# Performance work log

Hardware: AMD Instinct MI355X
Metric: run time of the kernel (lower is better)

Reference implementation:

```python
import jax, jax.numpy as jnp
import numpy as np

BS, N_PER, EMBED, ENC, L, OUT = 8, 8192, 128, 512, 512, 256
N = BS * N_PER          # total batched nodes
E_PER = 131072          # edges per graph (avg degree 16)
N_HE = 4096             # number of hyperedges (global over batched graph)
P = 1048576             # hyperedge incidence pairs


def _lin(k, i, o):
    return (jax.random.normal(k, (i, o), jnp.float32) / np.sqrt(i)).astype(jnp.float32)


def setup_inputs() -> dict:
    key = jax.random.key(0)
    ks = jax.random.split(key, 16)
    x = jax.random.normal(ks[0], (BS, L, ENC), jnp.float32)
    node_features = jax.random.normal(ks[1], (BS, N_PER, EMBED), jnp.float32)
    # block-diagonal batched graph (dgl.batch semantics): edges stay within each graph
    off = (jnp.arange(BS, dtype=jnp.int32) * N_PER)[:, None]
    src = (jax.random.randint(ks[2], (BS, E_PER), 0, N_PER) + off).reshape(-1)
    dst = (jax.random.randint(ks[3], (BS, E_PER), 0, N_PER) + off).reshape(-1)
    edge_index = jnp.stack([src, dst])                      # [2, E]
    hn = jax.random.randint(ks[4], (P,), 0, N)              # incident node ids
    he = jax.random.randint(ks[5], (P,), 0, N_HE)           # incident hyperedge ids
    hyperedge_index = jnp.stack([hn, he], axis=1)           # [P, 2], transposed in forward like the torch code
    return {
        "x": x, "node_features": node_features,
        "edge_index": edge_index, "hyperedge_index": hyperedge_index,
        "Wg1": _lin(ks[6], EMBED, EMBED), "bg1": jnp.zeros((EMBED,), jnp.float32),
        "Wg2": _lin(ks[7], EMBED, EMBED), "bg2": jnp.zeros((EMBED,), jnp.float32),
        "Wh1": _lin(ks[8], EMBED, EMBED), "bh1": jnp.zeros((EMBED,), jnp.float32),
        "Wh2": _lin(ks[9], EMBED, EMBED), "bh2": jnp.zeros((EMBED,), jnp.float32),
        "Wm": _lin(ks[10], ENC, EMBED), "bm": jnp.zeros((EMBED,), jnp.float32),
        "Wm2": _lin(ks[11], EMBED, EMBED), "bm2": jnp.zeros((EMBED,), jnp.float32),
        "Ws": _lin(ks[12], ENC + EMBED, OUT // 2), "bs_": jnp.zeros((OUT // 2,), jnp.float32),
        "Wt": _lin(ks[13], ENC + EMBED, OUT // 2), "bt": jnp.zeros((OUT // 2,), jnp.float32),
    }


def _gconv(h, src, dst, W, b):
    # DGL GraphConv, norm='both', allow_zero_in_degree (degrees clamped to 1)
    ones = jnp.ones(src.shape, h.dtype)
    dout = jnp.maximum(jax.ops.segment_sum(ones, src, num_segments=N), 1.0)
    din = jnp.maximum(jax.ops.segment_sum(ones, dst, num_segments=N), 1.0)
    h = h * jax.lax.rsqrt(dout)[:, None]
    h = h @ W
    agg = jax.ops.segment_sum(h[src], dst, num_segments=N)
    return agg * jax.lax.rsqrt(din)[:, None] + b


def _hconv(h, pn, pe, W, b):
    # PyG HypergraphConv with hyperedge_weight=None (ones): X' = D^-1 H B^-1 H^T (X Theta) + bias
    h = h @ W
    ones = jnp.ones(pn.shape, h.dtype)
    D = jax.ops.segment_sum(ones, pn, num_segments=N)       # node hyper-degree
    B = jax.ops.segment_sum(ones, pe, num_segments=N_HE)    # hyperedge size
    Dinv = jnp.where(D > 0, 1.0 / D, 0.0)
    Binv = jnp.where(B > 0, 1.0 / B, 0.0)
    ef = Binv[:, None] * jax.ops.segment_sum(h[pn], pe, num_segments=N_HE)
    out = Dinv[:, None] * jax.ops.segment_sum(ef[pe], pn, num_segments=N)
    return out + b


def reference(x, node_features, edge_index, hyperedge_index,
              Wg1, bg1, Wg2, bg2, Wh1, bh1, Wh2, bh2,
              Wm, bm, Wm2, bm2, Ws, bs_, Wt, bt):
    src, dst = edge_index[0], edge_index[1]
    hidx = hyperedge_index.T                 # matches torch .transpose(0, 1)
    pn, pe = hidx[0], hidx[1]
    nfr = node_features.reshape(N, EMBED)    # concatenated per-graph node features

    h = _gconv(nfr, src, dst, Wg1, bg1)
    h = _hconv(h, pn, pe, Wh1, bh1)
    h = jax.nn.relu(h) + nfr
    h = _gconv(h, src, dst, Wg2, bg2)
    h = _hconv(h, pn, pe, Wh2, bh2)
    h = jax.nn.relu(h) + nfr

    g = h.reshape(BS, N_PER, EMBED)          # equal node counts -> pad/split is a reshape
    q = jax.nn.relu(x @ Wm + bm)             # [BS, L, EMBED]
    k = jax.nn.relu(jnp.einsum('bnd,de->bne', g, Wm2) + bm2)
    C = jnp.einsum('bld,bnd->bln', q, k)     # cross-attention scores
    H = jnp.einsum('bln,bnd->bld', jax.nn.softmax(C, axis=2), g)
    cat = jnp.concatenate([x, H], axis=2)    # [BS, L, ENC+EMBED]
    G1 = jax.nn.sigmoid(cat @ Ws + bs_)
    G2 = jnp.tanh(cat @ Wt + bt)
    return jnp.concatenate([G1, G2], axis=2)  # [BS, L, OUT], dropout is identity at eval
```

## Files before the change

kernel.cpp:

```cpp
#include <hip/hip_runtime.h>
#include <hip/hip_bf16.h>

#define BSZ   8
#define NPER  8192
#define NNODE 65536
#define EPG   131072
#define EMB   128
#define ENCD  512
#define LQ    512
#define NHE   4096
#define NE    1048576
#define NP    1048576
#define NROW  4096
#define NSPLIT 16
#define SLOT_N 64
#define SLOT_E 384
#define CAP_E  10240
#define CAP_PN 10240
#define CAP_PE 18432

typedef _Float16 f16;
typedef _Float16 f16x2 __attribute__((ext_vector_type(2)));
typedef _Float16 f16x4 __attribute__((ext_vector_type(4)));
typedef _Float16 f16x8 __attribute__((ext_vector_type(8)));
typedef float f32x4 __attribute__((ext_vector_type(4)));
typedef unsigned short u16;
typedef unsigned int u32;

__global__ __launch_bounds__(256) void k_bin(const int* __restrict__ eidx,
    const int* __restrict__ hidx, int* __restrict__ gcur,
    u32* __restrict__ bin_e, u32* __restrict__ bin_s,
    u32* __restrict__ bin_pn, u32* __restrict__ bin_pe)
{
  __shared__ int lh[448];
  __shared__ int gb[448];
  const int tid = threadIdx.x;
  for (int i = tid; i < 448; i += 256) lh[i] = 0;
  __syncthreads();
  if (blockIdx.x < 256){
    const int eb4 = blockIdx.x*1024;
    int ss[16], dd[16];
    #pragma unroll
    for (int t = 0; t < 4; ++t){
      int4 s4 = ((const int4*)eidx)[eb4 + t*256 + tid];
      int4 d4 = ((const int4*)(eidx + NE))[eb4 + t*256 + tid];
      ss[t*4+0]=s4.x; ss[t*4+1]=s4.y; ss[t*4+2]=s4.z; ss[t*4+3]=s4.w;
      dd[t*4+0]=d4.x; dd[t*4+1]=d4.y; dd[t*4+2]=d4.z; dd[t*4+3]=d4.w;
    }
    int rd[16], rs[16];
    #pragma unroll
    for (int u = 0; u < 16; ++u){
      rd[u] = atomicAdd(&lh[dd[u] >> 9], 1);
      rs[u] = atomicAdd(&lh[128 + (ss[u] >> 9)], 1);
    }
    __syncthreads();
    if (tid < 128){
      if (lh[tid]) gb[tid] = atomicAdd(&gcur[tid], lh[tid]);
    } else {
      if (lh[tid]) gb[tid] = atomicAdd(&gcur[192 + tid], lh[tid]);
    }
    __syncthreads();
    #pragma unroll
    for (int u = 0; u < 16; ++u){
      int b = dd[u] >> 9;
      int pos = gb[b] + rd[u];
      if (pos < CAP_E)
        bin_e[(size_t)b*CAP_E + pos] = (u32)(dd[u] & 0xffff) | ((u32)ss[u] << 16);
      int bs = ss[u] >> 9;
      int pos2 = gb[128 + bs] + rs[u];
      if (pos2 < CAP_E)
        bin_s[(size_t)bs*CAP_E + pos2] = (u32)(ss[u] & 0xffff);
    }
  } else {
    const int pb4 = (blockIdx.x - 256)*2048;
    int pn[16], pe[16];
    #pragma unroll
    for (int t = 0; t < 8; ++t){
      int4 p = ((const int4*)hidx)[pb4 + t*256 + tid];
      pn[t*2+0] = p.x; pe[t*2+0] = p.y;
      pn[t*2+1] = p.z; pe[t*2+1] = p.w;
    }
    int rn[16], re[16];
    #pragma unroll
    for (int u = 0; u < 16; ++u){
      rn[u] = atomicAdd(&lh[128 + (pn[u] >> 9)], 1);
      re[u] = atomicAdd(&lh[256 + (pe[u] >> 6)], 1);
    }
    __syncthreads();
    if (tid < 192 && lh[128 + tid]) gb[128 + tid] = atomicAdd(&gcur[128 + tid], lh[128 + tid]);
    __syncthreads();
    #pragma unroll
    for (int u = 0; u < 16; ++u){
      int bn = pn[u] >> 9;
      int pos = gb[128 + bn] + rn[u];
      if (pos < CAP_PN)
        bin_pn[(size_t)bn*CAP_PN + pos] = (u32)pn[u] | ((u32)pe[u] << 16);
      int be = pe[u] >> 6;
      int pos2 = gb[256 + be] + re[u];
      if (pos2 < CAP_PE)
        bin_pe[(size_t)be*CAP_PE + pos2] = (u32)pe[u] | ((u32)pn[u] << 16);
    }
  }
}

__global__ __launch_bounds__(256) void k_csr(const int* __restrict__ gcur,
    const u32* __restrict__ bin_e, const u32* __restrict__ bin_s,
    const u32* __restrict__ bin_pn, const u32* __restrict__ bin_pe,
    int* __restrict__ cnt_dst, u16* __restrict__ csr_dst,
    int* __restrict__ cnt_pn, u16* __restrict__ csr_pn,
    int* __restrict__ cnt_pe, u16* __restrict__ csr_pe,
    int* __restrict__ du)
{
  const int tid = threadIdx.x;
  if (blockIdx.x < 256){
    __shared__ int cur[512];
    const int isP = blockIdx.x >= 128;
    const int b = blockIdx.x & 127;
    cur[tid] = 0; cur[tid + 256] = 0;
    __syncthreads();
    const int n0 = b*512;
    const int cap = isP ? CAP_PN : CAP_E;
    int raw = gcur[isP ? 128 + b : b];
    int count = raw < cap ? raw : cap;
    const u32* bin = (isP ? bin_pn : bin_e) + (size_t)b*cap;
    u16* csr = isP ? csr_pn : csr_dst;
    for (int i = tid; i < count; i += 256){
      u32 v = bin[i];
      int row = v & 0xffff, val = v >> 16;
      int c = atomicAdd(&cur[row - n0], 1);
      if (c < SLOT_N) csr[(size_t)row*SLOT_N + c] = (u16)val;
    }
    __syncthreads();
    int* cnt = isP ? cnt_pn : cnt_dst;
    cnt[n0 + tid]       = cur[tid];
    cnt[n0 + 256 + tid] = cur[tid + 256];
  } else if (blockIdx.x < 320){
    __shared__ int cur[64];
    const int b = blockIdx.x - 256;
    if (tid < 64) cur[tid] = 0;
    __syncthreads();
    const int e0 = b*64;
    int raw = gcur[256 + b];
    int count = raw < CAP_PE ? raw : CAP_PE;
    const u32* bin = bin_pe + (size_t)b*CAP_PE;
    for (int i = tid; i < count; i += 256){
      u32 v = bin[i];
      int row = v & 0xffff, val = v >> 16;
      int c = atomicAdd(&cur[row - e0], 1);
      if (c < SLOT_E) csr_pe[(size_t)row*SLOT_E + c] = (u16)val;
    }
    __syncthreads();
    if (tid < 64) cnt_pe[e0 + tid] = cur[tid];
  } else {
    __shared__ int cur[512];
    const int b = blockIdx.x - 320;
    cur[tid] = 0; cur[tid + 256] = 0;
    __syncthreads();
    const int n0 = b*512;
    int raw = gcur[320 + b];
    int count = raw < CAP_E ? raw : CAP_E;
    const u32* bin = bin_s + (size_t)b*CAP_E;
    for (int i = tid; i < count; i += 256){
      int row = (int)(bin[i] & 0xffff);
      atomicAdd(&cur[row - n0], 1);
    }
    __syncthreads();
    du[n0 + tid]       = cur[tid];
    du[n0 + 256 + tid] = cur[tid + 256];
  }
}

__global__ __launch_bounds__(256) void k_wprep(const float* __restrict__ Wg1,
    const float* __restrict__ Wg2, const float* __restrict__ Wm2,
    f16* __restrict__ wg1, f16* __restrict__ wg2, f16* __restrict__ wm2)
{
  int id = blockIdx.x*256 + threadIdx.x;
  int wsel = id >> 12;
  int r = id & 4095;
  int n = r >> 5, k0 = (r & 31)*4;
  const float* src = (wsel == 0 ? Wg1 : wsel == 1 ? Wg2 : Wm2) + n;
  f16* dst = wsel == 0 ? wg1 : wsel == 1 ? wg2 : wm2;
  f16x4 o = { (f16)src[(k0+0)*128], (f16)src[(k0+1)*128],
              (f16)src[(k0+2)*128], (f16)src[(k0+3)*128] };
  *(f16x4*)(dst + n*128 + k0) = o;
}

__global__ __launch_bounds__(256) void k_pre(const float* __restrict__ nfr,
    const int* __restrict__ du, f16* __restrict__ out)
{
  int i = blockIdx.x*256 + threadIdx.x;
  int node = i >> 6, j = i & 63;
  float ds = rsqrtf(fmaxf((float)du[node], 1.f));
  float2 v = ((const float2*)(nfr + (size_t)node*128))[j];
  f16x2 o = { (f16)(v.x*ds), (f16)(v.y*ds) };
  ((f16x2*)(out + (size_t)node*128))[j] = o;
}

__global__ __launch_bounds__(256) void k_gagg16(const int* __restrict__ cnt,
    const u16* __restrict__ csr, const f16* __restrict__ src, f16* __restrict__ agg)
{
  const int wv = threadIdx.x >> 6, lane = threadIdx.x & 63;
  const int blk = blockIdx.x;
  const int n = (blk & 7)*NPER + (blk >> 3)*4 + wv;
  const int nd = cnt[n];
  const int c = nd < SLOT_N ? nd : SLOT_N;
  const u16* row = csr + (size_t)n*SLOT_N;
  const f16x2* s2 = (const f16x2*)src;
  float ax = 0.f, ay = 0.f;
  if (c > 0){
    const int i0 = row[0];
    #pragma unroll 1
    for (int b = 0; b < 8; ++b){
      if (b*8 >= c) break;
      int4 iv = *(const int4*)(row + b*8);
      int ix[8] = { iv.x & 0xffff, (iv.x >> 16) & 0xffff,
                    iv.y & 0xffff, (iv.y >> 16) & 0xffff,
                    iv.z & 0xffff, (iv.z >> 16) & 0xffff,
                    iv.w & 0xffff, (iv.w >> 16) & 0xffff };
      f16x2 vv[8];
      #pragma unroll
      for (int k = 0; k < 8; ++k){
        int id = (b*8 + k < c) ? ix[k] : i0;
        vv[k] = s2[(size_t)id*64 + lane];
      }
      #pragma unroll
      for (int k = 0; k < 8; ++k){
        if (b*8 + k < c){ ax += (float)vv[k].x; ay += (float)vv[k].y; }
      }
    }
  }
  ((f16x2*)(agg + (size_t)n*128))[lane] = (f16x2){ (f16)ax, (f16)ay };
}

__global__ __launch_bounds__(256) void k_hea16(const int* __restrict__ cnt,
    const u16* __restrict__ csr, const f16* __restrict__ src, float* __restrict__ ef)
{
  const int wv = threadIdx.x >> 6, lane = threadIdx.x & 63;
  const int e = blockIdx.x*4 + wv;
  const int nd = cnt[e];
  const int n = nd < SLOT_E ? nd : SLOT_E;
  const u16* row = csr + (size_t)e*SLOT_E;
  const f16x2* s2 = (const f16x2*)src;
  float ax = 0.f, ay = 0.f;
  int j = 0;
  for (; j + 7 < n; j += 8){
    int p0 = row[j],   p1 = row[j+1], p2 = row[j+2], p3 = row[j+3];
    int p4 = row[j+4], p5 = row[j+5], p6 = row[j+6], p7 = row[j+7];
    f16x2 v0 = s2[(size_t)p0*64 + lane];
    f16x2 v1 = s2[(size_t)p1*64 + lane];
    f16x2 v2 = s2[(size_t)p2*64 + lane];
    f16x2 v3 = s2[(size_t)p3*64 + lane];
    f16x2 v4 = s2[(size_t)p4*64 + lane];
    f16x2 v5 = s2[(size_t)p5*64 + lane];
    f16x2 v6 = s2[(size_t)p6*64 + lane];
    f16x2 v7 = s2[(size_t)p7*64 + lane];
    ax += (((float)v0.x + (float)v1.x) + ((float)v2.x + (float)v3.x))
        + (((float)v4.x + (float)v5.x) + ((float)v6.x + (float)v7.x));
    ay += (((float)v0.y + (float)v1.y) + ((float)v2.y + (float)v3.y))
        + (((float)v4.y + (float)v5.y) + ((float)v6.y + (float)v7.y));
  }
  for (; j < n; ++j){
    f16x2 v = s2[(size_t)row[j]*64 + lane];
    ax += (float)v.x; ay += (float)v.y;
  }
  float s = nd > 0 ? 1.f/(float)nd : 0.f;
  ((float2*)(ef + (size_t)e*128))[lane] = make_float2(ax*s, ay*s);
}

template<int MODE>
__global__ __launch_bounds__(256) void k_ngemm(const f16* __restrict__ inp,
    const f16* __restrict__ wT, const int* __restrict__ cnt,
    const float* __restrict__ bias, f16* __restrict__ outp)
{
  const int wv = threadIdx.x >> 6, lane = threadIdx.x & 63;
  const int quad = lane >> 4, col = lane & 15;
  const int koff = quad*8;
  const int row0 = blockIdx.x*64 + wv*16;
  const f16* ar = inp + (size_t)(row0 + col)*128 + koff;
  const f16* br = wT + (size_t)col*128 + koff;
  f32x4 acc[8];
  #pragma unroll
  for (int nt = 0; nt < 8; ++nt) acc[nt] = (f32x4){0.f,0.f,0.f,0.f};
  #pragma unroll
  for (int ks = 0; ks < 4; ++ks){
    f16x8 a = *(const f16x8*)(ar + ks*32);
    #pragma unroll
    for (int nt = 0; nt < 8; ++nt){
      f16x8 b = *(const f16x8*)(br + (size_t)nt*16*128 + ks*32);
      acc[nt] = __builtin_amdgcn_mfma_f32_16x16x32_f16(a, b, acc[nt], 0, 0, 0);
    }
  }
  float sc[4];
  #pragma unroll
  for (int r = 0; r < 4; ++r)
    sc[r] = (MODE == 1) ? rsqrtf(fmaxf((float)cnt[row0 + quad*4 + r], 1.f)) : 1.f;
  #pragma unroll
  for (int nt = 0; nt < 8; ++nt){
    int n = nt*16 + col;
    float bv = bias[n];
    #pragma unroll
    for (int r = 0; r < 4; ++r){
      float v = acc[nt][r];
      if (MODE == 1) v = v*sc[r] + bv;
      else           v = fmaxf(v + bv, 0.f);
      outp[(size_t)(row0 + quad*4 + r)*128 + n] = (f16)v;
    }
  }
}

template<int MODE, int IN16>
__global__ __launch_bounds__(256, 2) void k_gemm(const void* __restrict__ inp,
    const float* __restrict__ W, const int* __restrict__ cnt,
    const float* __restrict__ bias, void* __restrict__ outp)
{
  __shared__ float Wl[128*128];
  __shared__ float Rl[32*128];
  const int tid = threadIdx.x;
  const int rbase = blockIdx.x*32;
  for (int i = tid; i < 16384; i += 256) Wl[i] = W[i];
  if (IN16){
    const f16x2* s2 = (const f16x2*)(((const f16*)inp) + (size_t)rbase*128);
    for (int i = tid; i < 2048; i += 256){
      f16x2 v = s2[i];
      ((float2*)Rl)[i] = make_float2((float)v.x, (float)v.y);
    }
  } else {
    const float* src = ((const float*)inp) + (size_t)rbase*128;
    for (int i = tid; i < 4096; i += 256) Rl[i] = src[i];
  }
  __syncthreads();
  const int c0 = (tid & 31)*4;
  const int r0 = (tid >> 5)*4;
  f32x4 acc[4];
  #pragma unroll
  for (int j = 0; j < 4; ++j) acc[j] = (f32x4){0.f,0.f,0.f,0.f};
  for (int d = 0; d < 128; d += 4){
    f32x4 w0 = *(const f32x4*)&Wl[(d+0)*128 + c0];
    f32x4 w1 = *(const f32x4*)&Wl[(d+1)*128 + c0];
    f32x4 w2 = *(const f32x4*)&Wl[(d+2)*128 + c0];
    f32x4 w3 = *(const f32x4*)&Wl[(d+3)*128 + c0];
    #pragma unroll
    for (int j = 0; j < 4; ++j){
      f32x4 rr = *(const f32x4*)&Rl[(r0+j)*128 + d];
      acc[j] += rr.x*w0 + rr.y*w1 + rr.z*w2 + rr.w*w3;
    }
  }
  #pragma unroll
  for (int j = 0; j < 4; ++j){
    const int row = rbase + r0 + j;
    if (MODE == 0){
      *(f32x4*)(((float*)outp) + (size_t)row*128 + c0) = acc[j];
    } else if (MODE == 1){
      float sc = rsqrtf(fmaxf((float)cnt[row], 1.f));
      f16* o = ((f16*)outp) + (size_t)row*128 + c0;
      #pragma unroll
      for (int k = 0; k < 4; ++k) o[k] = (f16)(acc[j][k]*sc + bias[c0+k]);
    } else if (MODE == 2){
      f16* o = ((f16*)outp) + (size_t)row*128 + c0;
      #pragma unroll
      for (int k = 0; k < 4; ++k) o[k] = (f16)fmaxf(acc[j][k] + bias[c0+k], 0.f);
    } else {
      f16* o = ((f16*)outp) + (size_t)row*128 + c0;
      #pragma unroll
      for (int k = 0; k < 4; ++k) o[k] = (f16)acc[j][k];
    }
  }
}

template<int PRES>
__global__ __launch_bounds__(256) void k_nha(const int* __restrict__ cnt,
    const u16* __restrict__ csr, const f16* __restrict__ ef,
    const float* __restrict__ bias, const float* __restrict__ nfr,
    const int* __restrict__ du, f16* __restrict__ outp)
{
  const int wv = threadIdx.x >> 6, lane = threadIdx.x & 63;
  const int n = blockIdx.x*4 + wv;
  const int nd = cnt[n];
  const int c = nd < SLOT_N ? nd : SLOT_N;
  const u16* row = csr + (size_t)n*SLOT_N;
  const f16x2* s2 = (const f16x2*)ef;
  float2 nf = ((const float2*)(nfr + (size_t)n*128))[lane];
  float e0 = PRES ? rsqrtf(fmaxf((float)du[n], 1.f)) : 1.f;
  float ax = 0.f, ay = 0.f;
  if (c > 0){
    const int i0 = row[0];
    #pragma unroll 1
    for (int b = 0; b < 8; ++b){
      if (b*8 >= c) break;
      int4 iv = *(const int4*)(row + b*8);
      int ix[8] = { iv.x & 0xffff, (iv.x >> 16) & 0xffff,
                    iv.y & 0xffff, (iv.y >> 16) & 0xffff,
                    iv.z & 0xffff, (iv.z >> 16) & 0xffff,
                    iv.w & 0xffff, (iv.w >> 16) & 0xffff };
      f16x2 vv[8];
      #pragma unroll
      for (int k = 0; k < 8; ++k){
        int id = (b*8 + k < c) ? ix[k] : i0;
        vv[k] = s2[(size_t)id*64 + lane];
      }
      #pragma unroll
      for (int k = 0; k < 8; ++k){
        if (b*8 + k < c){ ax += (float)vv[k].x; ay += (float)vv[k].y; }
      }
    }
  }
  float bx = bias[lane*2], by = bias[lane*2+1];
  float s = nd > 0 ? 1.f/(float)nd : 0.f;
  float vx = fmaxf(ax*s + bx, 0.f) + nf.x;
  float vy = fmaxf(ay*s + by, 0.f) + nf.y;
  ((f16x2*)(outp + (size_t)n*128))[lane] = (f16x2){ (f16)(vx*e0), (f16)(vy*e0) };
}

__global__ __launch_bounds__(256) void k_gt(const f16* __restrict__ g, f16* __restrict__ gT)
{
  __shared__ f16 t[64][66];
  int b = blockIdx.z, n0 = blockIdx.x*64, c0 = blockIdx.y*64;
  for (int i = threadIdx.x; i < 64*64; i += 256){
    int n = i >> 6, c = i & 63;
    t[n][c] = g[((size_t)(b*NPER + n0 + n))*128 + c0 + c];
  }
  __syncthreads();
  for (int i = threadIdx.x; i < 64*64; i += 256){
    int c = i >> 6, n = i & 63;
    gT[((size_t)(b*128 + c0 + c))*NPER + n0 + n] = t[n][c];
  }
}

#define NCH 64
__global__ __launch_bounds__(512, 4) void k_flash(const f16* __restrict__ qb,
    const f16* __restrict__ kb, const f16* __restrict__ gT,
    f16* __restrict__ Opart, float* __restrict__ mZ)
{
  __shared__ f16 Kl[64*128];
  __shared__ f16 Vl[128*64];
  __shared__ f16 Pl[8*16*64];
  const int sp = blockIdx.x, l0 = blockIdx.y*128, b = blockIdx.z;
  const int tid = threadIdx.x;
  const int w = tid >> 6, lane = tid & 63;
  const int quad = lane >> 4, col = lane & 15;
  const int koff = quad*8;
  const int krow = tid >> 4;
  const int kc8  = tid & 15;
  const int vrow = tid >> 3;
  const int vc8  = tid & 7;

  const f16* qrow = qb + ((size_t)(b*LQ + l0 + w*16 + col))*128 + koff;
  f16x8 aq[4];
  #pragma unroll
  for (int ks = 0; ks < 4; ++ks) aq[ks] = *(const f16x8*)(qrow + ks*32);
  float mrun[4] = {-1e30f,-1e30f,-1e30f,-1e30f};
  float zrun[4] = {0.f,0.f,0.f,0.f};
  f32x4 O[8];
  #pragma unroll
  for (int i = 0; i < 8; ++i) O[i] = (f32x4){0.f,0.f,0.f,0.f};

  const int nbase = sp*(NPER/NSPLIT);
  f16x8 kr[2], vr[2];
#define LOADKV(N0)                                                           \
  { _Pragma("unroll")                                                        \
    for (int i2 = 0; i2 < 2; ++i2){                                          \
      kr[i2] = *(const f16x8*)(kb + ((size_t)(b*NPER + (N0) + krow + i2*32))*128 + kc8*8); \
      vr[i2] = *(const f16x8*)(gT + ((size_t)(b*128 + vrow + i2*64))*NPER + (N0) + vc8*8); \
    } }
  LOADKV(nbase);
  #pragma unroll 1
  for (int it = 0; it < (NPER/NSPLIT)/NCH; ++it){
    const int n0 = nbase + it*NCH;
    __syncthreads();
    #pragma unroll
    for (int i2 = 0; i2 < 2; ++i2){
      int r = krow + i2*32;
      *(f16x8*)&Kl[r*128 + ((kc8 ^ (r & 7))*8)] = kr[i2];
      int d = vrow + i2*64;
      *(f16x8*)&Vl[d*64  + ((vc8 ^ (d & 7))*8)] = vr[i2];
    }
    __syncthreads();
    if (it < (NPER/NSPLIT)/NCH - 1) LOADKV(n0 + NCH);

    f32x4 st[4];
    #pragma unroll
    for (int t = 0; t < 4; ++t){
      st[t] = (f32x4){0.f,0.f,0.f,0.f};
      const int r = t*16 + col, rs = r & 7;
      #pragma unroll
      for (int ks = 0; ks < 4; ++ks){
        f16x8 bf = *(const f16x8*)&Kl[r*128 + (((ks*4 + quad) ^ rs)*8)];
        st[t] = __builtin_amdgcn_mfma_f32_16x16x32_f16(aq[ks], bf, st[t], 0, 0, 0);
      }
    }
    float alr[4];
    #pragma unroll
    for (int r = 0; r < 4; ++r){
      float rm = st[0][r];
      #pragma unroll
      for (int t = 1; t < 4; ++t) rm = fmaxf(rm, st[t][r]);
      rm = fmaxf(rm, __shfl_xor(rm, 1));
      rm = fmaxf(rm, __shfl_xor(rm, 2));
      rm = fmaxf(rm, __shfl_xor(rm, 4));
      rm = fmaxf(rm, __shfl_xor(rm, 8));
      float mn = fmaxf(mrun[r], rm);
      float al = __expf(mrun[r] - mn);
      float ps[4], rsum = 0.f;
      #pragma unroll
      for (int t = 0; t < 4; ++t){ ps[t] = __expf(st[t][r] - mn); rsum += ps[t]; }
      rsum += __shfl_xor(rsum, 1);
      rsum += __shfl_xor(rsum, 2);
      rsum += __shfl_xor(rsum, 4);
      rsum += __shfl_xor(rsum, 8);
      zrun[r] = zrun[r]*al + rsum;
      mrun[r] = mn;
      alr[r] = al;
      const int prow = quad*4 + r, pswz = prow & 7;
      #pragma unroll
      for (int t = 0; t < 4; ++t)
        Pl[w*1024 + prow*64 + (((t*2 + (col >> 3)) ^ pswz)*8) + (col & 7)] = (f16)ps[t];
    }
    #pragma unroll
    for (int dt = 0; dt < 8; ++dt)
      #pragma unroll
      for (int r = 0; r < 4; ++r) O[dt][r] *= alr[r];
    __builtin_amdgcn_wave_barrier();
    #pragma unroll
    for (int kk = 0; kk < 2; ++kk){
      f16x8 ap = *(const f16x8*)&Pl[w*1024 + col*64 + (((kk*4 + quad) ^ (col & 7))*8)];
      #pragma unroll
      for (int dt = 0; dt < 8; ++dt){
        const int d = col + dt*16;
        f16x8 bv = *(const f16x8*)&Vl[d*64 + (((kk*4 + quad) ^ (d & 7))*8)];
        O[dt] = __builtin_amdgcn_mfma_f32_16x16x32_f16(ap, bv, O[dt], 0, 0, 0);
      }
    }
    __builtin_amdgcn_wave_barrier();
  }
#undef LOADKV
  const int growb = b*LQ + l0 + w*16 + quad*4;
  #pragma unroll
  for (int r = 0; r < 4; ++r){
    f16* od = Opart + ((size_t)sp*NROW + growb + r)*128 + col;
    #pragma unroll
    for (int dt = 0; dt < 8; ++dt) od[dt*16] = (f16)O[dt][r];
  }
  if (col == 0){
    #pragma unroll
    for (int r = 0; r < 4; ++r){
      ((float2*)mZ)[(size_t)sp*NROW + growb + r] = make_float2(mrun[r], zrun[r]);
    }
  }
}

__global__ __launch_bounds__(256) void k_comb(const f16* __restrict__ Opart,
    const float* __restrict__ mZ, f16* __restrict__ cat)
{
  int i = blockIdx.x*256 + threadIdx.x;
  int row = i >> 6, d2 = (i & 63)*2;
  float ms[NSPLIT], zs[NSPLIT];
  float M = -1e30f;
  #pragma unroll
  for (int s = 0; s < NSPLIT; ++s){
    float2 v = ((const float2*)mZ)[(size_t)s*NROW + row];
    ms[s] = v.x; zs[s] = v.y;
    M = fmaxf(M, v.x);
  }
  float Zt = 0.f, ax = 0.f, ay = 0.f;
  #pragma unroll
  for (int s = 0; s < NSPLIT; ++s){
    float e = __expf(ms[s] - M);
    Zt += zs[s]*e;
    f16x2 op = *(const f16x2*)(Opart + ((size_t)s*NROW + row)*128 + d2);
    ax += e*(float)op.x; ay += e*(float)op.y;
  }
  float inv = 1.f/Zt;
  f16x2 o = { (f16)(ax*inv), (f16)(ay*inv) };
  *(f16x2*)(cat + (size_t)row*640 + 512 + d2) = o;
}

__global__ __launch_bounds__(256) void k_prep(const float* __restrict__ x,
    const float* __restrict__ Wsg, const float* __restrict__ Wtn,
    const float* __restrict__ Wm,
    f16* __restrict__ cat, f16* __restrict__ w16, f16* __restrict__ wm16)
{
  if (blockIdx.x < 2048){
    int id = blockIdx.x*256 + threadIdx.x;
    int row = id >> 7, c4 = (id & 127)*4;
    float4 v = *(const float4*)(x + (size_t)row*512 + c4);
    f16x4 o = { (f16)v.x, (f16)v.y, (f16)v.z, (f16)v.w };
    *(f16x4*)(cat + (size_t)row*640 + c4) = o;
  } else if (blockIdx.x < 2208){
    int id = (blockIdx.x - 2048)*256 + threadIdx.x;
    int n = id / 160;
    int k0 = (id - n*160)*4;
    const float* src = n < 128 ? (Wsg + n) : (Wtn + (n - 128));
    f16x4 o = { (f16)src[(k0+0)*128], (f16)src[(k0+1)*128],
                (f16)src[(k0+2)*128], (f16)src[(k0+3)*128] };
    *(f16x4*)(w16 + (size_t)n*640 + k0) = o;
  } else {
    int id = (blockIdx.x - 2208)*256 + threadIdx.x;
    int n = id >> 7;
    int k0 = (id & 127)*4;
    const float* src = Wm + n;
    f16x4 o = { (f16)src[(k0+0)*128], (f16)src[(k0+1)*128],
                (f16)src[(k0+2)*128], (f16)src[(k0+3)*128] };
    *(f16x4*)(wm16 + (size_t)n*512 + k0) = o;
  }
}

__global__ __launch_bounds__(64) void k_qgemm2(const f16* __restrict__ cat,
    const f16* __restrict__ wm16, const float* __restrict__ bm, f16* __restrict__ q)
{
  const int lane = threadIdx.x;
  const int quad = lane >> 4, col = lane & 15;
  const int koff = quad*8;
  const int row0 = blockIdx.x * 16;
  const f16* ar = cat + (size_t)(row0 + col)*640 + koff;
  const f16* br = wm16 + (size_t)col*512 + koff;
  f32x4 acc[8];
  #pragma unroll
  for (int nt = 0; nt < 8; ++nt) acc[nt] = (f32x4){0.f,0.f,0.f,0.f};
  for (int ks = 0; ks < 16; ++ks){
    f16x8 a = *(const f16x8*)(ar + ks*32);
    #pragma unroll
    for (int nt = 0; nt < 8; ++nt){
      f16x8 b = *(const f16x8*)(br + (size_t)nt*16*512 + ks*32);
      acc[nt] = __builtin_amdgcn_mfma_f32_16x16x32_f16(a, b, acc[nt], 0, 0, 0);
    }
  }
  #pragma unroll
  for (int nt = 0; nt < 8; ++nt){
    int n = nt*16 + col;
    float bv = bm[n];
    #pragma unroll
    for (int r = 0; r < 4; ++r){
      float v = fmaxf(acc[nt][r] + bv, 0.f);
      q[(size_t)(row0 + quad*4 + r)*128 + n] = (f16)v;
    }
  }
}

__global__ __launch_bounds__(64) void k_fin2(const f16* __restrict__ cat,
    const f16* __restrict__ w16, const float* __restrict__ bsg,
    const float* __restrict__ btn, float* __restrict__ out)
{
  const int lane = threadIdx.x;
  const int quad = lane >> 4, col = lane & 15;
  const int koff = quad*8;
  const int row0 = blockIdx.x * 16;
  const f16* ar = cat + (size_t)(row0 + col)*640 + koff;
  const f16* br = w16 + (size_t)col*640 + koff;
  f32x4 acc[16];
  #pragma unroll
  for (int nt = 0; nt < 16; ++nt) acc[nt] = (f32x4){0.f,0.f,0.f,0.f};
  for (int ks = 0; ks < 20; ++ks){
    f16x8 a = *(const f16x8*)(ar + ks*32);
    #pragma unroll
    for (int nt = 0; nt < 16; ++nt){
      f16x8 b = *(const f16x8*)(br + (size_t)nt*16*640 + ks*32);
      acc[nt] = __builtin_amdgcn_mfma_f32_16x16x32_f16(a, b, acc[nt], 0, 0, 0);
    }
  }
  #pragma unroll
  for (int nt = 0; nt < 16; ++nt){
    int n = nt*16 + col;
    float bv = n < 128 ? bsg[n] : btn[n - 128];
    #pragma unroll
    for (int r = 0; r < 4; ++r){
      float v = acc[nt][r] + bv;
      v = n < 128 ? 1.f/(1.f + __expf(-v)) : tanhf(v);
      out[(size_t)(row0 + quad*4 + r)*256 + n] = v;
    }
  }
}

extern "C" void kernel_launch(void* const* d_in, const int* in_sizes, int n_in,
                              void* d_out, int out_size, void* d_ws, size_t ws_size,
                              hipStream_t stream)
{
  const float* x    = (const float*)d_in[0];
  const float* nfr  = (const float*)d_in[1];
  const int*   eidx = (const int*)d_in[2];
  const int*   hidx = (const int*)d_in[3];
  const float *Wg1=(const float*)d_in[4],  *bg1=(const float*)d_in[5];
  const float *Wg2=(const float*)d_in[6],  *bg2=(const float*)d_in[7];
  const float *Wh1=(const float*)d_in[8],  *bh1=(const float*)d_in[9];
  const float *Wh2=(const float*)d_in[10], *bh2=(const float*)d_in[11];
  const float *Wm =(const float*)d_in[12], *bm =(const float*)d_in[13];
  const float *Wm2=(const float*)d_in[14], *bm2=(const float*)d_in[15];
  const float *Wsg=(const float*)d_in[16], *bsg=(const float*)d_in[17];
  const float *Wtn=(const float*)d_in[18], *btn=(const float*)d_in[19];
  float* out = (float*)d_out;

  char* base = (char*)d_ws;
  f16*   h4_16  = (f16*)(base);
  f16*   agg16  = (f16*)(base + 33554432);
  u32*   bin_e  = (u32*)(base + 33554432);
  u32*   bin_pn = (u32*)(base + 38797312);
  u32*   bin_pe = (u32*)(base + 44040192);
  int*   gcur   = (int*)(base + 48758784);
  u32*   bin_s  = (u32*)(base + 50331648);
  f16*   wg1_16 = (f16*)(base + 55574528);
  f16*   wg2_16 = (f16*)(base + 55607296);
  f16*   wm2_16 = (f16*)(base + 55640064);
  f16*   cat16  = (f16*)(base + 33554432);
  f16*   w16    = (f16*)(base + 38797312);
  f16*   wm16   = (f16*)(base + 39124992);
  f16*   bufA   = (f16*)(base + 67108864);
  f16*   bufB   = (f16*)(base + 83886080);
  f16*   Opart  = (f16*)(base + 67108864);
  u16*   csr_dst= (u16*)(base + 100663296);
  f16*   kb     = (f16*)(base + 100663296);
  u16*   csr_pn = (u16*)(base + 117440512);
  f16*   gT     = (f16*)(base + 117440512);
  u16*   csr_pe = (u16*)(base + 134217728);
  int*   cnt_dst= (int*)(base + 140509184);
  int*   cnt_pn = (int*)(base + 140771328);
  int*   cnt_pe = (int*)(base + 141033472);
  int*   du     = (int*)(base + 141049856);
  float* ef0    = (float*)(base + 141312000);
  f16*   ef1    = (f16*)(base + 143409152);
  f16*   qb     = (f16*)(base + 145506304);
  float* mZ     = (float*)(base + 146554880);
  const size_t needB = (size_t)147079168;
  if (ws_size < needB) return;

  hipMemsetAsync(gcur, 0, 1792, stream);
  k_wprep<<<48, 256, 0, stream>>>(Wg1, Wg2, Wm2, wg1_16, wg2_16, wm2_16);
  k_bin<<<512, 256, 0, stream>>>(eidx, hidx, gcur, bin_e, bin_s, bin_pn, bin_pe);
  k_csr<<<448, 256, 0, stream>>>(gcur, bin_e, bin_s, bin_pn, bin_pe,
                                 cnt_dst, csr_dst, cnt_pn, csr_pn, cnt_pe, csr_pe, du);

  k_pre<<<NNODE*64/256, 256, 0, stream>>>(nfr, du, bufA);
  k_gagg16<<<NNODE/4, 256, 0, stream>>>(cnt_dst, csr_dst, bufA, agg16);
  k_ngemm<1><<<NNODE/64, 256, 0, stream>>>(agg16, wg1_16, cnt_dst, bg1, bufB);
  k_hea16<<<NHE/4, 256, 0, stream>>>(cnt_pe, csr_pe, bufB, ef0);
  k_gemm<3,0><<<NHE/32, 256, 0, stream>>>(ef0, Wh1, nullptr, nullptr, ef1);
  k_nha<1><<<NNODE/4, 256, 0, stream>>>(cnt_pn, csr_pn, ef1, bh1, nfr, du, bufA);

  k_gagg16<<<NNODE/4, 256, 0, stream>>>(cnt_dst, csr_dst, bufA, agg16);
  k_ngemm<1><<<NNODE/64, 256, 0, stream>>>(agg16, wg2_16, cnt_dst, bg2, bufB);
  k_hea16<<<NHE/4, 256, 0, stream>>>(cnt_pe, csr_pe, bufB, ef0);
  k_gemm<3,0><<<NHE/32, 256, 0, stream>>>(ef0, Wh2, nullptr, nullptr, ef1);
  k_nha<0><<<NNODE/4, 256, 0, stream>>>(cnt_pn, csr_pn, ef1, bh2, nfr, nullptr, h4_16);

  k_prep<<<2272, 256, 0, stream>>>(x, Wsg, Wtn, Wm, cat16, w16, wm16);
  k_qgemm2<<<NROW/16, 64, 0, stream>>>(cat16, wm16, bm, qb);
  k_ngemm<2><<<NNODE/64, 256, 0, stream>>>(h4_16, wm2_16, nullptr, bm2, kb);
  k_gt<<<dim3(NPER/64, 2, BSZ), 256, 0, stream>>>(h4_16, gT);
  k_flash<<<dim3(NSPLIT, LQ/128, BSZ), 512, 0, stream>>>(qb, kb, gT, Opart, mZ);
  k_comb<<<NROW*64/256, 256, 0, stream>>>(Opart, mZ, cat16);
  k_fin2<<<NROW/16, 64, 0, stream>>>(cat16, w16, bsg, btn, out);

  (void)in_sizes; (void)n_in; (void)out_size;
}
```

Measured before the change: 550.1 us.

## Give each flash wave two query row groups and fold log2e into q

The flash-attention kernel drops from 512 to 256 threads per block, and each wave now handles 32 query rows as two 16-row groups. Every K and V fragment read from LDS then feeds two MFMAs, which doubles register-level reuse and halves the number of waves per tile. Separately, q is pre-scaled by log2(e) in the q GEMM, so the softmax and the split combine can use exp2f instead of __expf. The price is much higher register pressure from doubled accumulators and a lower launch-bounds occupancy target.

```diff
diff --git a/kernel.cpp b/kernel.cpp
--- a/kernel.cpp
+++ b/kernel.cpp
@@ -427,7 +427,7 @@
 }
 
 #define NCH 64
-__global__ __launch_bounds__(512, 4) void k_flash(const f16* __restrict__ qb,
+__global__ __launch_bounds__(256, 2) void k_flash(const f16* __restrict__ qb,
     const f16* __restrict__ kb, const f16* __restrict__ gT,
     f16* __restrict__ Opart, float* __restrict__ mZ)
 {
@@ -444,23 +444,31 @@
   const int vrow = tid >> 3;
   const int vc8  = tid & 7;
 
-  const f16* qrow = qb + ((size_t)(b*LQ + l0 + w*16 + col))*128 + koff;
-  f16x8 aq[4];
-  #pragma unroll
-  for (int ks = 0; ks < 4; ++ks) aq[ks] = *(const f16x8*)(qrow + ks*32);
-  float mrun[4] = {-1e30f,-1e30f,-1e30f,-1e30f};
-  float zrun[4] = {0.f,0.f,0.f,0.f};
-  f32x4 O[8];
-  #pragma unroll
-  for (int i = 0; i < 8; ++i) O[i] = (f32x4){0.f,0.f,0.f,0.f};
+  f16x8 aq[2][4];
+  #pragma unroll
+  for (int g = 0; g < 2; ++g){
+    const f16* qrow = qb + ((size_t)(b*LQ + l0 + w*32 + g*16 + col))*128 + koff;
+    #pragma unroll
+    for (int ks = 0; ks < 4; ++ks) aq[g][ks] = *(const f16x8*)(qrow + ks*32);
+  }
+  float mrun[2][4], zrun[2][4];
+  #pragma unroll
+  for (int g = 0; g < 2; ++g)
+    #pragma unroll
+    for (int r = 0; r < 4; ++r){ mrun[g][r] = -1e30f; zrun[g][r] = 0.f; }
+  f32x4 O[2][8];
+  #pragma unroll
+  for (int g = 0; g < 2; ++g)
+    #pragma unroll
+    for (int i = 0; i < 8; ++i) O[g][i] = (f32x4){0.f,0.f,0.f,0.f};
 
   const int nbase = sp*(NPER/NSPLIT);
-  f16x8 kr[2], vr[2];
+  f16x8 kr[4], vr[4];
 #define LOADKV(N0)                                                           \
   { _Pragma("unroll")                                                        \
-    for (int i2 = 0; i2 < 2; ++i2){                                          \
-      kr[i2] = *(const f16x8*)(kb + ((size_t)(b*NPER + (N0) + krow + i2*32))*128 + kc8*8); \
-      vr[i2] = *(const f16x8*)(gT + ((size_t)(b*128 + vrow + i2*64))*NPER + (N0) + vc8*8); \
+    for (int i2 = 0; i2 < 4; ++i2){                                          \
+      kr[i2] = *(const f16x8*)(kb + ((size_t)(b*NPER + (N0) + krow + i2*16))*128 + kc8*8); \
+      vr[i2] = *(const f16x8*)(gT + ((size_t)(b*128 + vrow + i2*32))*NPER + (N0) + vc8*8); \
     } }
   LOADKV(nbase);
   #pragma unroll 1
@@ -468,82 +476,92 @@
     const int n0 = nbase + it*NCH;
     __syncthreads();
     #pragma unroll
-    for (int i2 = 0; i2 < 2; ++i2){
-      int r = krow + i2*32;
+    for (int i2 = 0; i2 < 4; ++i2){
+      int r = krow + i2*16;
       *(f16x8*)&Kl[r*128 + ((kc8 ^ (r & 7))*8)] = kr[i2];
-      int d = vrow + i2*64;
+      int d = vrow + i2*32;
       *(f16x8*)&Vl[d*64  + ((vc8 ^ (d & 7))*8)] = vr[i2];
     }
     __syncthreads();
     if (it < (NPER/NSPLIT)/NCH - 1) LOADKV(n0 + NCH);
 
-    f32x4 st[4];
+    f32x4 st[2][4];
     #pragma unroll
     for (int t = 0; t < 4; ++t){
-      st[t] = (f32x4){0.f,0.f,0.f,0.f};
+      st[0][t] = (f32x4){0.f,0.f,0.f,0.f};
+      st[1][t] = (f32x4){0.f,0.f,0.f,0.f};
       const int r = t*16 + col, rs = r & 7;
       #pragma unroll
       for (int ks = 0; ks < 4; ++ks){
         f16x8 bf = *(const f16x8*)&Kl[r*128 + (((ks*4 + quad) ^ rs)*8)];
-        st[t] = __builtin_amdgcn_mfma_f32_16x16x32_f16(aq[ks], bf, st[t], 0, 0, 0);
+        st[0][t] = __builtin_amdgcn_mfma_f32_16x16x32_f16(aq[0][ks], bf, st[0][t], 0, 0, 0);
+        st[1][t] = __builtin_amdgcn_mfma_f32_16x16x32_f16(aq[1][ks], bf, st[1][t], 0, 0, 0);
       }
     }
-    float alr[4];
-    #pragma unroll
-    for (int r = 0; r < 4; ++r){
-      float rm = st[0][r];
-      #pragma unroll
-      for (int t = 1; t < 4; ++t) rm = fmaxf(rm, st[t][r]);
-      rm = fmaxf(rm, __shfl_xor(rm, 1));
-      rm = fmaxf(rm, __shfl_xor(rm, 2));
-      rm = fmaxf(rm, __shfl_xor(rm, 4));
-      rm = fmaxf(rm, __shfl_xor(rm, 8));
-      float mn = fmaxf(mrun[r], rm);
-      float al = __expf(mrun[r] - mn);
-      float ps[4], rsum = 0.f;
-      #pragma unroll
-      for (int t = 0; t < 4; ++t){ ps[t] = __expf(st[t][r] - mn); rsum += ps[t]; }
-      rsum += __shfl_xor(rsum, 1);
-      rsum += __shfl_xor(rsum, 2);
-      rsum += __shfl_xor(rsum, 4);
-      rsum += __shfl_xor(rsum, 8);
-      zrun[r] = zrun[r]*al + rsum;
-      mrun[r] = mn;
-      alr[r] = al;
-      const int prow = quad*4 + r, pswz = prow & 7;
-      #pragma unroll
-      for (int t = 0; t < 4; ++t)
-        Pl[w*1024 + prow*64 + (((t*2 + (col >> 3)) ^ pswz)*8) + (col & 7)] = (f16)ps[t];
-    }
-    #pragma unroll
-    for (int dt = 0; dt < 8; ++dt)
-      #pragma unroll
-      for (int r = 0; r < 4; ++r) O[dt][r] *= alr[r];
+    float alr[2][4];
+    #pragma unroll
+    for (int g = 0; g < 2; ++g){
+      #pragma unroll
+      for (int r = 0; r < 4; ++r){
+        float rm = st[g][0][r];
+        #pragma unroll
+        for (int t = 1; t < 4; ++t) rm = fmaxf(rm, st[g][t][r]);
+        rm = fmaxf(rm, __shfl_xor(rm, 1));
+        rm = fmaxf(rm, __shfl_xor(rm, 2));
+        rm = fmaxf(rm, __shfl_xor(rm, 4));
+        rm = fmaxf(rm, __shfl_xor(rm, 8));
+        float mn = fmaxf(mrun[g][r], rm);
+        float al = exp2f(mrun[g][r] - mn);
+        float ps[4], rsum = 0.f;
+        #pragma unroll
+        for (int t = 0; t < 4; ++t){ ps[t] = exp2f(st[g][t][r] - mn); rsum += ps[t]; }
+        rsum += __shfl_xor(rsum, 1);
+        rsum += __shfl_xor(rsum, 2);
+        rsum += __shfl_xor(rsum, 4);
+        rsum += __shfl_xor(rsum, 8);
+        zrun[g][r] = zrun[g][r]*al + rsum;
+        mrun[g][r] = mn;
+        alr[g][r] = al;
+        const int prow = quad*4 + r, pswz = prow & 7;
+        #pragma unroll
+        for (int t = 0; t < 4; ++t)
+          Pl[(w*2+g)*1024 + prow*64 + (((t*2 + (col >> 3)) ^ pswz)*8) + (col & 7)] = (f16)ps[t];
+      }
+      #pragma unroll
+      for (int dt = 0; dt < 8; ++dt)
+        #pragma unroll
+        for (int r = 0; r < 4; ++r) O[g][dt][r] *= alr[g][r];
+    }
     __builtin_amdgcn_wave_barrier();
     #pragma unroll
     for (int kk = 0; kk < 2; ++kk){
-      f16x8 ap = *(const f16x8*)&Pl[w*1024 + col*64 + (((kk*4 + quad) ^ (col & 7))*8)];
+      f16x8 ap0 = *(const f16x8*)&Pl[(w*2+0)*1024 + col*64 + (((kk*4 + quad) ^ (col & 7))*8)];
+      f16x8 ap1 = *(const f16x8*)&Pl[(w*2+1)*1024 + col*64 + (((kk*4 + quad) ^ (col & 7))*8)];
       #pragma unroll
       for (int dt = 0; dt < 8; ++dt){
         const int d = col + dt*16;
         f16x8 bv = *(const f16x8*)&Vl[d*64 + (((kk*4 + quad) ^ (d & 7))*8)];
-        O[dt] = __builtin_amdgcn_mfma_f32_16x16x32_f16(ap, bv, O[dt], 0, 0, 0);
+        O[0][dt] = __builtin_amdgcn_mfma_f32_16x16x32_f16(ap0, bv, O[0][dt], 0, 0, 0);
+        O[1][dt] = __builtin_amdgcn_mfma_f32_16x16x32_f16(ap1, bv, O[1][dt], 0, 0, 0);
       }
     }
     __builtin_amdgcn_wave_barrier();
   }
 #undef LOADKV
-  const int growb = b*LQ + l0 + w*16 + quad*4;
-  #pragma unroll
-  for (int r = 0; r < 4; ++r){
-    f16* od = Opart + ((size_t)sp*NROW + growb + r)*128 + col;
-    #pragma unroll
-    for (int dt = 0; dt < 8; ++dt) od[dt*16] = (f16)O[dt][r];
-  }
-  if (col == 0){
+  #pragma unroll
+  for (int g = 0; g < 2; ++g){
+    const int growb = b*LQ + l0 + w*32 + g*16 + quad*4;
     #pragma unroll
     for (int r = 0; r < 4; ++r){
-      ((float2*)mZ)[(size_t)sp*NROW + growb + r] = make_float2(mrun[r], zrun[r]);
+      f16* od = Opart + ((size_t)sp*NROW + growb + r)*128 + col;
+      #pragma unroll
+      for (int dt = 0; dt < 8; ++dt) od[dt*16] = (f16)O[g][dt][r];
+    }
+    if (col == 0){
+      #pragma unroll
+      for (int r = 0; r < 4; ++r){
+        ((float2*)mZ)[(size_t)sp*NROW + growb + r] = make_float2(mrun[g][r], zrun[g][r]);
+      }
     }
   }
 }
@@ -564,7 +582,7 @@
   float Zt = 0.f, ax = 0.f, ay = 0.f;
   #pragma unroll
   for (int s = 0; s < NSPLIT; ++s){
-    float e = __expf(ms[s] - M);
+    float e = exp2f(ms[s] - M);
     Zt += zs[s]*e;
     f16x2 op = *(const f16x2*)(Opart + ((size_t)s*NROW + row)*128 + d2);
     ax += e*(float)op.x; ay += e*(float)op.y;
@@ -630,7 +648,7 @@
     float bv = bm[n];
     #pragma unroll
     for (int r = 0; r < 4; ++r){
-      float v = fmaxf(acc[nt][r] + bv, 0.f);
+      float v = fmaxf(acc[nt][r] + bv, 0.f) * 1.44269504f;
       q[(size_t)(row0 + quad*4 + r)*128 + n] = (f16)v;
     }
   }
@@ -744,7 +762,7 @@
   k_qgemm2<<<NROW/16, 64, 0, stream>>>(cat16, wm16, bm, qb);
   k_ngemm<2><<<NNODE/64, 256, 0, stream>>>(h4_16, wm2_16, nullptr, bm2, kb);
   k_gt<<<dim3(NPER/64, 2, BSZ), 256, 0, stream>>>(h4_16, gT);
-  k_flash<<<dim3(NSPLIT, LQ/128, BSZ), 512, 0, stream>>>(qb, kb, gT, Opart, mZ);
+  k_flash<<<dim3(NSPLIT, LQ/128, BSZ), 256, 0, stream>>>(qb, kb, gT, Opart, mZ);
   k_comb<<<NROW*64/256, 256, 0, stream>>>(Opart, mZ, cat16);
   k_fin2<<<NROW/16, 64, 0, stream>>>(cat16, w16, bsg, btn, out);
 
```

Measured after the change: 559.4 us. No clear change (+1.7%).
